# Optimization experiments

Hardware: AMD Instinct MI355X
Metric: run time of the kernel (lower is better)

Reference implementation:

```python
import jax, jax.numpy as jnp
import numpy as np

B, S, D, H = 4, 2048, 1024, 16
HD = D // H

def _linear_params(key, fan_in, fan_out):
    kw, kb = jax.random.split(key)
    bound = 1.0 / np.sqrt(fan_in)
    W = jax.random.uniform(kw, (fan_in, fan_out), minval=-bound, maxval=bound, dtype=jnp.float32)
    b = jax.random.uniform(kb, (fan_out,), minval=-bound, maxval=bound, dtype=jnp.float32)
    return W, b

def setup_inputs() -> dict:
    key = jax.random.key(0)
    ks = jax.random.split(key, 7)
    query = jax.random.normal(ks[0], (B, S, D), dtype=jnp.float32)
    key_t = jax.random.normal(ks[1], (B, S, D), dtype=jnp.float32)
    value = jax.random.normal(ks[2], (B, S, D), dtype=jnp.float32)
    Wq, bq = _linear_params(ks[3], D, D)
    Wk, bk = _linear_params(ks[4], D, D)
    Wv, bv = _linear_params(ks[5], D, D)
    Wo, bo = _linear_params(ks[6], D, D)
    return {"query": query, "key": key_t, "value": value,
            "Wq": Wq, "bq": bq, "Wk": Wk, "bk": bk,
            "Wv": Wv, "bv": bv, "Wo": Wo, "bo": bo}

def reference(query, key, value, Wq, bq, Wk, bk, Wv, bv, Wo, bo):
    b, s, _ = query.shape
    scale = HD ** -0.5
    # project and split heads -> [b, h, s, hd]
    Q = (query @ Wq + bq).reshape(b, s, H, HD).transpose(0, 2, 1, 3)
    K = (key @ Wk + bk).reshape(b, s, H, HD).transpose(0, 2, 1, 3)
    V = (value @ Wv + bv).reshape(b, s, H, HD).transpose(0, 2, 1, 3)
    scores = jnp.einsum('bhqd,bhkd->bhqk', Q, K) * scale  # [b,h,s,s]
    attn = jax.nn.softmax(scores, axis=-1)
    out = jnp.einsum('bhqk,bhkd->bhqd', attn, V)
    out = out.transpose(0, 2, 1, 3).reshape(b, s, D)
    return out @ Wo + bo
```

## Files before the change

### kernel.cpp

```cpp
#include <hip/hip_runtime.h>

typedef unsigned short u16;
typedef __attribute__((ext_vector_type(8))) short short8;
typedef __attribute__((ext_vector_type(4))) float f32x4;
typedef __attribute__((ext_vector_type(4))) unsigned int u32x4;

union V8 { u32x4 u; short8 s; };

__device__ __forceinline__ u16 f2bf(float f) {
  union { float f; unsigned u; } v; v.f = f;
  unsigned r = v.u + 0x7fffu + ((v.u >> 16) & 1u);
  return (u16)(r >> 16);
}

__device__ __forceinline__ unsigned cvt_pk_bf16(float lo, float hi) {
  unsigned r;
  asm("v_cvt_pk_bf16_f32 %0, %1, %2" : "=v"(r) : "v"(lo), "v"(hi));
  return r;
}

__device__ __forceinline__ void gload_lds16(const void* g, void* l) {
  __builtin_amdgcn_global_load_lds((const __attribute__((address_space(1))) unsigned int*)g,
                                   (__attribute__((address_space(3))) unsigned int*)l, 16, 0, 0);
}

__device__ __forceinline__ f32x4 mfma16(short8 a, short8 b, f32x4 c) {
  return __builtin_amdgcn_mfma_f32_16x16x32_bf16(a, b, c, 0, 0, 0);
}

__global__ __launch_bounds__(256) void wtrans4_kernel(const float* __restrict__ Wq, const float* __restrict__ Wk,
                                                      const float* __restrict__ Wv, const float* __restrict__ Wo,
                                                      u16* __restrict__ WtQ, u16* __restrict__ WtK,
                                                      u16* __restrict__ WtV, u16* __restrict__ WtO) {
  const int bid = blockIdx.x;
  const int wsel = bid >> 9;
  const float* W = (wsel == 0) ? Wq : (wsel == 1) ? Wk : (wsel == 2) ? Wv : Wo;
  u16* Wt = (wsel == 0) ? WtQ : (wsel == 1) ? WtK : (wsel == 2) ? WtV : WtO;
  const int tid = (bid & 511) * 256 + threadIdx.x;
  const int n = tid & 1023;
  const int kb = (tid >> 10) << 3;
  u32x4 w;
#pragma unroll
  for (int j = 0; j < 4; j++)
    w[j] = cvt_pk_bf16(W[(size_t)(kb + 2 * j) * 1024 + n], W[(size_t)(kb + 2 * j + 1) * 1024 + n]);
  *(u32x4*)(Wt + (size_t)n * 1024 + kb) = w;
}

__global__ __launch_bounds__(256) void gemm_qkv_kernel(const float* __restrict__ Aq,
                                                       const float* __restrict__ Ak,
                                                       const float* __restrict__ Av,
                                                       const u16* __restrict__ Wt,
                                                       const float* __restrict__ bq,
                                                       const float* __restrict__ bk,
                                                       const float* __restrict__ bv,
                                                       u16* __restrict__ Outs,
                                                       float qscale) {
  constexpr int K = 1024;
  __shared__ u16 Ash[2][4096];
  __shared__ u16 Bsh[2][4096];
  const int t = threadIdx.x;
  const int l = t & 63;
  const int w = t >> 6;
  const int wm = w >> 1, wn = w & 1;
  const int bid0 = blockIdx.x;
  const int swz = (bid0 & 7) * 192 + (bid0 >> 3);
  const int bm = swz >> 3, bn = swz & 7;
  const int sec = bm >> 6;
  const int m0 = (bm & 63) * 128, n0 = bn * 128;
  const float* Asrc = (sec == 0) ? Aq : (sec == 1) ? Ak : Av;
  const u16* Bb = Wt + ((size_t)sec << 20) + (size_t)n0 * K;

  f32x4 acc[4][4];
#pragma unroll
  for (int i = 0; i < 4; i++)
#pragma unroll
    for (int j = 0; j < 4; j++) acc[i][j] = (f32x4){0.f, 0.f, 0.f, 0.f};

  const int line0 = t >> 3, c8 = t & 7;
  const int lc0 = c8 ^ (line0 & 7);
  const int row0 = 2 * line0 + (lc0 >> 2);
  const int kc0 = (lc0 & 3) << 3;
  const int line1 = line0 + 32;
  const int lc1 = c8 ^ (line1 & 7);
  const int row1 = 2 * line1 + (lc1 >> 2);
  const int kc1 = (lc1 & 3) << 3;

  const float* A0 = Asrc + (size_t)(m0 + row0) * K + kc0;
  const float* A1 = Asrc + (size_t)(m0 + row1) * K + kc1;

  int aoff[4], boff[4];
#pragma unroll
  for (int mt = 0; mt < 4; mt++) {
    int R = wm * 64 + mt * 16 + (l & 15);
    int cc = (((R & 1) << 2) + (l >> 4)) ^ ((R >> 1) & 7);
    aoff[mt] = (R >> 1) * 64 + cc * 8;
  }
#pragma unroll
  for (int nt = 0; nt < 4; nt++) {
    int R = wn * 64 + nt * 16 + (l & 15);
    int cc = (((R & 1) << 2) + (l >> 4)) ^ ((R >> 1) & 7);
    boff[nt] = (R >> 1) * 64 + cc * 8;
  }

  float4 La0, La1, La2, La3;
  auto loadA = [&](int k0) {
    La0 = *(const float4*)(A0 + k0);
    La1 = *(const float4*)(A0 + k0 + 4);
    La2 = *(const float4*)(A1 + k0);
    La3 = *(const float4*)(A1 + k0 + 4);
  };
  auto writeA = [&](int buf) {
    u32x4 w0, w1;
    w0[0] = cvt_pk_bf16(La0.x, La0.y); w0[1] = cvt_pk_bf16(La0.z, La0.w);
    w0[2] = cvt_pk_bf16(La1.x, La1.y); w0[3] = cvt_pk_bf16(La1.z, La1.w);
    w1[0] = cvt_pk_bf16(La2.x, La2.y); w1[1] = cvt_pk_bf16(La2.z, La2.w);
    w1[2] = cvt_pk_bf16(La3.x, La3.y); w1[3] = cvt_pk_bf16(La3.z, La3.w);
    *(u32x4*)&Ash[buf][t * 8] = w0;
    *(u32x4*)&Ash[buf][2048 + t * 8] = w1;
  };
  auto stB = [&](int buf, int k0) {
    u16* BW = &Bsh[buf][w * 512];
    gload_lds16(Bb + (size_t)row0 * K + k0 + kc0, BW);
    gload_lds16(Bb + (size_t)row1 * K + k0 + kc1, BW + 2048);
  };

  loadA(0);
  stB(0, 0);
  writeA(0);
  __syncthreads();

  int cur = 0;
  for (int k0 = 0; k0 < K; k0 += 32) {
    const bool nxt = (k0 + 32 < K);
    if (nxt) { loadA(k0 + 32); stB(cur ^ 1, k0 + 32); }
    short8 af[4], bfr[4];
#pragma unroll
    for (int mt = 0; mt < 4; mt++) af[mt] = *(const short8*)&Ash[cur][aoff[mt]];
#pragma unroll
    for (int nt = 0; nt < 4; nt++) bfr[nt] = *(const short8*)&Bsh[cur][boff[nt]];
    __builtin_amdgcn_s_setprio(1);
#pragma unroll
    for (int mt = 0; mt < 4; mt++)
#pragma unroll
      for (int nt = 0; nt < 4; nt++)
        acc[mt][nt] = mfma16(af[mt], bfr[nt], acc[mt][nt]);
    __builtin_amdgcn_s_setprio(0);
    if (nxt) writeA(cur ^ 1);
    __syncthreads();
    cur ^= 1;
  }

#pragma unroll
  for (int nt = 0; nt < 4; nt++) {
    const int n = n0 + wn * 64 + nt * 16 + (l & 15);
    const float bias = (sec == 0) ? bq[n] : (sec == 1) ? bk[n] : bv[n];
    if (sec < 2) {
      const float outscale = (sec == 0) ? qscale : 1.0f;
      u16* C = Outs + ((size_t)sec << 23);
#pragma unroll
      for (int mt = 0; mt < 4; mt++) {
        const int m = m0 + wm * 64 + mt * 16 + ((l >> 4) << 2);
#pragma unroll
        for (int r = 0; r < 4; r++)
          C[(size_t)(m + r) * 1024 + n] = f2bf((acc[mt][nt][r] + bias) * outscale);
      }
    } else {
      const int b2 = m0 >> 11;
      const int h2 = n >> 6, d = n & 63;
      u16* C = Outs + ((size_t)2 << 23);
#pragma unroll
      for (int mt = 0; mt < 4; mt++) {
        const int s0 = (m0 & 2047) + wm * 64 + mt * 16 + ((l >> 4) << 2);
        const int u = s0 & 63;
        const int pos = ((((u >> 2) & 3) + ((u >> 5) & 1) * 4) << 3) + ((u >> 4) & 1) * 4;
        const int sp = (s0 & ~63) + pos;
        ushort4 pk;
        pk.x = f2bf(acc[mt][nt][0] + bias);
        pk.y = f2bf(acc[mt][nt][1] + bias);
        pk.z = f2bf(acc[mt][nt][2] + bias);
        pk.w = f2bf(acc[mt][nt][3] + bias);
        *(ushort4*)(C + (((size_t)((b2 * 16 + h2) * 64 + d)) << 11) + sp) = pk;
      }
    }
  }
}

__global__ __launch_bounds__(256) void gemm_out_kernel(const u16* __restrict__ A,
                                                       const u16* __restrict__ Bt,
                                                       const float* __restrict__ bias,
                                                       float* __restrict__ Cout) {
  constexpr int K = 1024;
  __shared__ u16 Ash[2][4096];
  __shared__ u16 Bsh[2][4096];
  const int t = threadIdx.x;
  const int l = t & 63;
  const int w = t >> 6;
  const int wm = w >> 1, wn = w & 1;
  const int bid0 = blockIdx.x;
  const int swz = (bid0 & 7) * 64 + (bid0 >> 3);
  const int bm = swz >> 3, bn = swz & 7;
  const int m0 = bm * 128, n0 = bn * 128;

  f32x4 acc[4][4];
#pragma unroll
  for (int i = 0; i < 4; i++)
#pragma unroll
    for (int j = 0; j < 4; j++) acc[i][j] = (f32x4){0.f, 0.f, 0.f, 0.f};

  const int line0 = t >> 3, c8 = t & 7;
  const int lc0 = c8 ^ (line0 & 7);
  const int row0 = 2 * line0 + (lc0 >> 2);
  const int kc0 = (lc0 & 3) << 3;
  const int line1 = line0 + 32;
  const int lc1 = c8 ^ (line1 & 7);
  const int row1 = 2 * line1 + (lc1 >> 2);
  const int kc1 = (lc1 & 3) << 3;

  const u16* Ab = A + (size_t)m0 * K;
  const u16* Bb = Bt + (size_t)n0 * K;

  int aoff[4], boff[4];
#pragma unroll
  for (int mt = 0; mt < 4; mt++) {
    int R = wm * 64 + mt * 16 + (l & 15);
    int cc = (((R & 1) << 2) + (l >> 4)) ^ ((R >> 1) & 7);
    aoff[mt] = (R >> 1) * 64 + cc * 8;
  }
#pragma unroll
  for (int nt = 0; nt < 4; nt++) {
    int R = wn * 64 + nt * 16 + (l & 15);
    int cc = (((R & 1) << 2) + (l >> 4)) ^ ((R >> 1) & 7);
    boff[nt] = (R >> 1) * 64 + cc * 8;
  }

  auto stage = [&](int buf, int k0) {
    u16* AW = &Ash[buf][w * 512];
    u16* BW = &Bsh[buf][w * 512];
    gload_lds16(Ab + (size_t)row0 * K + k0 + kc0, AW);
    gload_lds16(Ab + (size_t)row1 * K + k0 + kc1, AW + 2048);
    gload_lds16(Bb + (size_t)row0 * K + k0 + kc0, BW);
    gload_lds16(Bb + (size_t)row1 * K + k0 + kc1, BW + 2048);
  };

  stage(0, 0);
  __syncthreads();
  int cur = 0;
  for (int k0 = 0; k0 < K; k0 += 32) {
    if (k0 + 32 < K) stage(cur ^ 1, k0 + 32);
    short8 af[4], bfr[4];
#pragma unroll
    for (int mt = 0; mt < 4; mt++) af[mt] = *(const short8*)&Ash[cur][aoff[mt]];
#pragma unroll
    for (int nt = 0; nt < 4; nt++) bfr[nt] = *(const short8*)&Bsh[cur][boff[nt]];
    __builtin_amdgcn_s_setprio(1);
#pragma unroll
    for (int mt = 0; mt < 4; mt++)
#pragma unroll
      for (int nt = 0; nt < 4; nt++)
        acc[mt][nt] = mfma16(af[mt], bfr[nt], acc[mt][nt]);
    __builtin_amdgcn_s_setprio(0);
    __syncthreads();
    cur ^= 1;
  }

#pragma unroll
  for (int nt = 0; nt < 4; nt++) {
    const int n = n0 + wn * 64 + nt * 16 + (l & 15);
    const float bv2 = bias[n];
#pragma unroll
    for (int mt = 0; mt < 4; mt++) {
      const int m = m0 + wm * 64 + mt * 16 + ((l >> 4) << 2);
#pragma unroll
      for (int r = 0; r < 4; r++)
        Cout[(size_t)(m + r) * 1024 + n] = acc[mt][nt][r] + bv2;
    }
  }
}

__device__ __forceinline__ void pack_half(const f32x4 (&s)[4], short8& pa0, short8& pa1) {
  float p[4][4];
#pragma unroll
  for (int c = 0; c < 4; c++)
#pragma unroll
    for (int r = 0; r < 4; r++) p[c][r] = __builtin_amdgcn_exp2f(s[c][r]);
  V8 u0, u1;
  u0.u[0] = cvt_pk_bf16(p[0][0], p[0][1]); u0.u[1] = cvt_pk_bf16(p[0][2], p[0][3]);
  u0.u[2] = cvt_pk_bf16(p[1][0], p[1][1]); u0.u[3] = cvt_pk_bf16(p[1][2], p[1][3]);
  u1.u[0] = cvt_pk_bf16(p[2][0], p[2][1]); u1.u[1] = cvt_pk_bf16(p[2][2], p[2][3]);
  u1.u[2] = cvt_pk_bf16(p[3][0], p[3][1]); u1.u[3] = cvt_pk_bf16(p[3][2], p[3][3]);
  pa0 = u0.s; pa1 = u1.s;
}

__global__ __launch_bounds__(256, 2) void attn_kernel(const u16* __restrict__ Qb,
                                                      const u16* __restrict__ Kb,
                                                      const u16* __restrict__ Vtb,
                                                      u16* __restrict__ AO) {
  __shared__ u16 Ksh[2][4096];
  __shared__ u16 Vsh[2][4096];
  const int t = threadIdx.x, l = t & 63, w = t >> 6;
  const int g = l >> 4, ql = l & 15;
  const int bid0 = blockIdx.x;
  const int bid = (bid0 & 7) * 64 + (bid0 >> 3);
  const int qt = bid & 7;
  const int bh = bid >> 3;
  const int h = bh & 15, b = bh >> 4;
  const int q0 = qt * 256 + w * 64;

  short8 qf[4][2];
#pragma unroll
  for (int hh = 0; hh < 4; hh++) {
    const u16* Qrow = Qb + ((size_t)b * 2048 + q0 + hh * 16 + ql) * 1024 + h * 64 + g * 8;
    qf[hh][0] = *(const short8*)(Qrow);
    qf[hh][1] = *(const short8*)(Qrow + 32);
  }

  f32x4 oacc[4][4];
  f32x4 lacc[4];
#pragma unroll
  for (int hh = 0; hh < 4; hh++) {
    lacc[hh] = (f32x4){0.f, 0.f, 0.f, 0.f};
#pragma unroll
    for (int dt = 0; dt < 4; dt++) oacc[hh][dt] = (f32x4){0.f, 0.f, 0.f, 0.f};
  }
  short8 ones;
#pragma unroll
  for (int i = 0; i < 8; i++) ones[i] = (short)0x3F80;

  const int srow0 = t >> 3, sc = t & 7;
  const int slc0 = sc ^ (srow0 & 7);
  const int srow1 = srow0 + 32, slc1 = sc ^ (srow1 & 7);
  const u16* Kbase = Kb + ((size_t)b * 2048) * 1024 + h * 64;
  const u16* Vbase = Vtb + ((size_t)(b * 16 + h) * 64) * 2048;

  auto stage = [&](int buf, int kk0) {
    u16* KW = &Ksh[buf][w * 512];
    u16* VW = &Vsh[buf][w * 512];
    gload_lds16(Kbase + (size_t)(kk0 + srow0) * 1024 + slc0 * 8, KW);
    gload_lds16(Kbase + (size_t)(kk0 + srow1) * 1024 + slc1 * 8, KW + 2048);
    gload_lds16(Vbase + (size_t)srow0 * 2048 + kk0 + slc0 * 8, VW);
    gload_lds16(Vbase + (size_t)srow1 * 2048 + kk0 + slc1 * 8, VW + 2048);
  };

  int voff0[4], voff1[4];
#pragma unroll
  for (int dt = 0; dt < 4; dt++) {
    const int d = dt * 16 + ql;
    voff0[dt] = d * 64 + ((g ^ (d & 7)) << 3);
    voff1[dt] = d * 64 + (((g + 4) ^ (d & 7)) << 3);
  }

  stage(0, 0);
  __syncthreads();
  int cur = 0;

  for (int kk0 = 0; kk0 < 2048; kk0 += 64) {
    if (kk0 + 64 < 2048) stage(cur ^ 1, kk0 + 64);
    const u16* KC = Ksh[cur];
    const u16* VC = Vsh[cur];

    f32x4 s[4][4];
    __builtin_amdgcn_s_setprio(1);
#pragma unroll
    for (int c = 0; c < 4; c++) {
      const int R = c * 16 + ql;
      const int x = R & 7;
      const short8 kf0 = *(const short8*)&KC[R * 64 + ((g ^ x) << 3)];
      const short8 kf1 = *(const short8*)&KC[R * 64 + (((g + 4) ^ x) << 3)];
#pragma unroll
      for (int hh = 0; hh < 4; hh++) {
        f32x4 z = (f32x4){0.f, 0.f, 0.f, 0.f};
        z = mfma16(kf0, qf[hh][0], z);
        s[hh][c] = mfma16(kf1, qf[hh][1], z);
      }
    }
    __builtin_amdgcn_s_setprio(0);

    short8 pa[4][2];
#pragma unroll
    for (int hh = 0; hh < 4; hh++) pack_half(s[hh], pa[hh][0], pa[hh][1]);

    __builtin_amdgcn_s_setprio(1);
#pragma unroll
    for (int hh = 0; hh < 4; hh++) {
      lacc[hh] = mfma16(pa[hh][0], ones, lacc[hh]);
      lacc[hh] = mfma16(pa[hh][1], ones, lacc[hh]);
    }
#pragma unroll
    for (int dt = 0; dt < 4; dt++) {
      const short8 vf0 = *(const short8*)&VC[voff0[dt]];
      const short8 vf1 = *(const short8*)&VC[voff1[dt]];
#pragma unroll
      for (int hh = 0; hh < 4; hh++) {
        oacc[hh][dt] = mfma16(pa[hh][0], vf0, oacc[hh][dt]);
        oacc[hh][dt] = mfma16(pa[hh][1], vf1, oacc[hh][dt]);
      }
    }
    __builtin_amdgcn_s_setprio(0);
    __syncthreads();
    cur ^= 1;
  }

#pragma unroll
  for (int hh = 0; hh < 4; hh++) {
    f32x4 inv;
#pragma unroll
    for (int r = 0; r < 4; r++) inv[r] = __builtin_amdgcn_rcpf(lacc[hh][r]);
    u16* Arow = AO + ((size_t)b * 2048 + q0 + hh * 16) * 1024 + h * 64;
#pragma unroll
    for (int dt = 0; dt < 4; dt++) {
      const int col = dt * 16 + ql;
#pragma unroll
      for (int r = 0; r < 4; r++)
        Arow[(size_t)(4 * g + r) * 1024 + col] = f2bf(oacc[hh][dt][r] * inv[r]);
    }
  }
}

extern "C" void kernel_launch(void* const* d_in, const int* in_sizes, int n_in,
                              void* d_out, int out_size, void* d_ws, size_t ws_size,
                              hipStream_t stream) {
  (void)in_sizes; (void)n_in; (void)out_size; (void)ws_size;
  const float* query = (const float*)d_in[0];
  const float* key   = (const float*)d_in[1];
  const float* value = (const float*)d_in[2];
  const float* Wq = (const float*)d_in[3];  const float* bq = (const float*)d_in[4];
  const float* Wk = (const float*)d_in[5];  const float* bk = (const float*)d_in[6];
  const float* Wv = (const float*)d_in[7];  const float* bv = (const float*)d_in[8];
  const float* Wo = (const float*)d_in[9];  const float* bo = (const float*)d_in[10];
  float* out = (float*)d_out;

  const size_t SZX = (size_t)8192 * 1024;
  const size_t SZW = (size_t)1024 * 1024;
  u16* AO  = (u16*)d_ws;
  u16* Qb  = AO + SZX;
  u16* Kbf = Qb + SZX;
  u16* Vtb = Kbf + SZX;
  u16* WtQ = Vtb + SZX;
  u16* WtK = WtQ + SZW;
  u16* WtV = WtK + SZW;
  u16* WtO = WtV + SZW;

  const float QSCALE = 0.125f * 1.44269504088896f;

  wtrans4_kernel<<<2048, 256, 0, stream>>>(Wq, Wk, Wv, Wo, WtQ, WtK, WtV, WtO);

  gemm_qkv_kernel<<<1536, 256, 0, stream>>>(query, key, value, WtQ, bq, bk, bv, Qb, QSCALE);

  attn_kernel<<<512, 256, 0, stream>>>(Qb, Kbf, Vtb, AO);

  gemm_out_kernel<<<512, 256, 0, stream>>>(AO, WtO, bo, out);
}
```

Baseline: 369.5 us.

## Pre-convert QKV activations to bf16 and stage GEMM A via direct LDS loads

Adds a prep pass that converts the fp32 query/key/value inputs to bf16 in workspace, fused with the weight transpose kernel. The QKV GEMM then loads A through global_load_lds like B, dropping the register round-trip and in-loop conversion. It also removes the s_setprio hints in both GEMMs. The cost is an extra full read and write of the activations (about 48MB read, 24MB write) before the GEMM, traded for a simpler, fully asynchronous GEMM pipeline.

```diff
diff --git a/kernel.cpp b/kernel.cpp
--- a/kernel.cpp
+++ b/kernel.cpp
@@ -28,27 +28,42 @@
   return __builtin_amdgcn_mfma_f32_16x16x32_bf16(a, b, c, 0, 0, 0);
 }
 
-__global__ __launch_bounds__(256) void wtrans4_kernel(const float* __restrict__ Wq, const float* __restrict__ Wk,
-                                                      const float* __restrict__ Wv, const float* __restrict__ Wo,
-                                                      u16* __restrict__ WtQ, u16* __restrict__ WtK,
-                                                      u16* __restrict__ WtV, u16* __restrict__ WtO) {
+__global__ __launch_bounds__(256) void prep_kernel(const float* __restrict__ q,
+                                                   const float* __restrict__ k,
+                                                   const float* __restrict__ v,
+                                                   const float* __restrict__ Wq, const float* __restrict__ Wk,
+                                                   const float* __restrict__ Wv, const float* __restrict__ Wo,
+                                                   u16* __restrict__ oq, u16* __restrict__ ok, u16* __restrict__ ov,
+                                                   u16* __restrict__ WtQ, u16* __restrict__ WtK,
+                                                   u16* __restrict__ WtV, u16* __restrict__ WtO) {
   const int bid = blockIdx.x;
-  const int wsel = bid >> 9;
-  const float* W = (wsel == 0) ? Wq : (wsel == 1) ? Wk : (wsel == 2) ? Wv : Wo;
-  u16* Wt = (wsel == 0) ? WtQ : (wsel == 1) ? WtK : (wsel == 2) ? WtV : WtO;
-  const int tid = (bid & 511) * 256 + threadIdx.x;
-  const int n = tid & 1023;
-  const int kb = (tid >> 10) << 3;
-  u32x4 w;
-#pragma unroll
-  for (int j = 0; j < 4; j++)
-    w[j] = cvt_pk_bf16(W[(size_t)(kb + 2 * j) * 1024 + n], W[(size_t)(kb + 2 * j + 1) * 1024 + n]);
-  *(u32x4*)(Wt + (size_t)n * 1024 + kb) = w;
-}
-
-__global__ __launch_bounds__(256) void gemm_qkv_kernel(const float* __restrict__ Aq,
-                                                       const float* __restrict__ Ak,
-                                                       const float* __restrict__ Av,
+  if (bid < 12288) {
+    const float* in = (bid < 4096) ? q : (bid < 8192 ? k : v);
+    u16* out = (bid < 4096) ? oq : (bid < 8192 ? ok : ov);
+    const size_t i = ((size_t)(bid & 4095) * 256 + threadIdx.x) * 8;
+    const float4* p = (const float4*)(in + i);
+    float4 a = p[0], b = p[1];
+    u32x4 w;
+    w[0] = cvt_pk_bf16(a.x, a.y); w[1] = cvt_pk_bf16(a.z, a.w);
+    w[2] = cvt_pk_bf16(b.x, b.y); w[3] = cvt_pk_bf16(b.z, b.w);
+    *(u32x4*)(out + i) = w;
+  } else {
+    const int wb = bid - 12288;
+    const int wsel = wb >> 9;
+    const float* W = (wsel == 0) ? Wq : (wsel == 1) ? Wk : (wsel == 2) ? Wv : Wo;
+    u16* Wt = (wsel == 0) ? WtQ : (wsel == 1) ? WtK : (wsel == 2) ? WtV : WtO;
+    const int tid = (wb & 511) * 256 + threadIdx.x;
+    const int n = tid & 1023;
+    const int kb = (tid >> 10) << 3;
+    u32x4 w;
+#pragma unroll
+    for (int j = 0; j < 4; j++)
+      w[j] = cvt_pk_bf16(W[(size_t)(kb + 2 * j) * 1024 + n], W[(size_t)(kb + 2 * j + 1) * 1024 + n]);
+    *(u32x4*)(Wt + (size_t)n * 1024 + kb) = w;
+  }
+}
+
+__global__ __launch_bounds__(256) void gemm_qkv_kernel(const u16* __restrict__ A,
                                                        const u16* __restrict__ Wt,
                                                        const float* __restrict__ bq,
                                                        const float* __restrict__ bk,
@@ -65,10 +80,11 @@
   const int bid0 = blockIdx.x;
   const int swz = (bid0 & 7) * 192 + (bid0 >> 3);
   const int bm = swz >> 3, bn = swz & 7;
-  const int sec = bm >> 6;
-  const int m0 = (bm & 63) * 128, n0 = bn * 128;
-  const float* Asrc = (sec == 0) ? Aq : (sec == 1) ? Ak : Av;
-  const u16* Bb = Wt + ((size_t)sec << 20) + (size_t)n0 * K;
+  const int m0 = bm * 128, n0 = bn * 128;
+  const int sec = m0 >> 13;
+  const u16* Bt = Wt + ((size_t)sec << 20);
+  const float* bias = (sec == 0) ? bq : (sec == 1) ? bk : bv;
+  const float outscale = (sec == 0) ? qscale : 1.0f;
 
   f32x4 acc[4][4];
 #pragma unroll
@@ -85,8 +101,8 @@
   const int row1 = 2 * line1 + (lc1 >> 2);
   const int kc1 = (lc1 & 3) << 3;
 
-  const float* A0 = Asrc + (size_t)(m0 + row0) * K + kc0;
-  const float* A1 = Asrc + (size_t)(m0 + row1) * K + kc1;
+  const u16* Ab = A + (size_t)m0 * K;
+  const u16* Bb = Bt + (size_t)n0 * K;
 
   int aoff[4], boff[4];
 #pragma unroll
@@ -102,50 +118,30 @@
     boff[nt] = (R >> 1) * 64 + cc * 8;
   }
 
-  float4 La0, La1, La2, La3;
-  auto loadA = [&](int k0) {
-    La0 = *(const float4*)(A0 + k0);
-    La1 = *(const float4*)(A0 + k0 + 4);
-    La2 = *(const float4*)(A1 + k0);
-    La3 = *(const float4*)(A1 + k0 + 4);
-  };
-  auto writeA = [&](int buf) {
-    u32x4 w0, w1;
-    w0[0] = cvt_pk_bf16(La0.x, La0.y); w0[1] = cvt_pk_bf16(La0.z, La0.w);
-    w0[2] = cvt_pk_bf16(La1.x, La1.y); w0[3] = cvt_pk_bf16(La1.z, La1.w);
-    w1[0] = cvt_pk_bf16(La2.x, La2.y); w1[1] = cvt_pk_bf16(La2.z, La2.w);
-    w1[2] = cvt_pk_bf16(La3.x, La3.y); w1[3] = cvt_pk_bf16(La3.z, La3.w);
-    *(u32x4*)&Ash[buf][t * 8] = w0;
-    *(u32x4*)&Ash[buf][2048 + t * 8] = w1;
-  };
-  auto stB = [&](int buf, int k0) {
+  auto stage = [&](int buf, int k0) {
+    u16* AW = &Ash[buf][w * 512];
     u16* BW = &Bsh[buf][w * 512];
+    gload_lds16(Ab + (size_t)row0 * K + k0 + kc0, AW);
+    gload_lds16(Ab + (size_t)row1 * K + k0 + kc1, AW + 2048);
     gload_lds16(Bb + (size_t)row0 * K + k0 + kc0, BW);
     gload_lds16(Bb + (size_t)row1 * K + k0 + kc1, BW + 2048);
   };
 
-  loadA(0);
-  stB(0, 0);
-  writeA(0);
+  stage(0, 0);
   __syncthreads();
-
   int cur = 0;
   for (int k0 = 0; k0 < K; k0 += 32) {
-    const bool nxt = (k0 + 32 < K);
-    if (nxt) { loadA(k0 + 32); stB(cur ^ 1, k0 + 32); }
+    if (k0 + 32 < K) stage(cur ^ 1, k0 + 32);
     short8 af[4], bfr[4];
 #pragma unroll
     for (int mt = 0; mt < 4; mt++) af[mt] = *(const short8*)&Ash[cur][aoff[mt]];
 #pragma unroll
     for (int nt = 0; nt < 4; nt++) bfr[nt] = *(const short8*)&Bsh[cur][boff[nt]];
-    __builtin_amdgcn_s_setprio(1);
 #pragma unroll
     for (int mt = 0; mt < 4; mt++)
 #pragma unroll
       for (int nt = 0; nt < 4; nt++)
         acc[mt][nt] = mfma16(af[mt], bfr[nt], acc[mt][nt]);
-    __builtin_amdgcn_s_setprio(0);
-    if (nxt) writeA(cur ^ 1);
     __syncthreads();
     cur ^= 1;
   }
@@ -153,32 +149,32 @@
 #pragma unroll
   for (int nt = 0; nt < 4; nt++) {
     const int n = n0 + wn * 64 + nt * 16 + (l & 15);
-    const float bias = (sec == 0) ? bq[n] : (sec == 1) ? bk[n] : bv[n];
+    const float bv2 = bias[n];
     if (sec < 2) {
-      const float outscale = (sec == 0) ? qscale : 1.0f;
       u16* C = Outs + ((size_t)sec << 23);
 #pragma unroll
       for (int mt = 0; mt < 4; mt++) {
-        const int m = m0 + wm * 64 + mt * 16 + ((l >> 4) << 2);
+        const int m = (m0 & 8191) + wm * 64 + mt * 16 + ((l >> 4) << 2);
 #pragma unroll
         for (int r = 0; r < 4; r++)
-          C[(size_t)(m + r) * 1024 + n] = f2bf((acc[mt][nt][r] + bias) * outscale);
+          C[(size_t)(m + r) * 1024 + n] = f2bf((acc[mt][nt][r] + bv2) * outscale);
       }
     } else {
-      const int b2 = m0 >> 11;
+      const int mloc = m0 & 8191;
+      const int b2 = mloc >> 11;
       const int h2 = n >> 6, d = n & 63;
       u16* C = Outs + ((size_t)2 << 23);
 #pragma unroll
       for (int mt = 0; mt < 4; mt++) {
-        const int s0 = (m0 & 2047) + wm * 64 + mt * 16 + ((l >> 4) << 2);
+        const int s0 = (mloc & 2047) + wm * 64 + mt * 16 + ((l >> 4) << 2);
         const int u = s0 & 63;
         const int pos = ((((u >> 2) & 3) + ((u >> 5) & 1) * 4) << 3) + ((u >> 4) & 1) * 4;
         const int sp = (s0 & ~63) + pos;
         ushort4 pk;
-        pk.x = f2bf(acc[mt][nt][0] + bias);
-        pk.y = f2bf(acc[mt][nt][1] + bias);
-        pk.z = f2bf(acc[mt][nt][2] + bias);
-        pk.w = f2bf(acc[mt][nt][3] + bias);
+        pk.x = f2bf(acc[mt][nt][0] + bv2);
+        pk.y = f2bf(acc[mt][nt][1] + bv2);
+        pk.z = f2bf(acc[mt][nt][2] + bv2);
+        pk.w = f2bf(acc[mt][nt][3] + bv2);
         *(ushort4*)(C + (((size_t)((b2 * 16 + h2) * 64 + d)) << 11) + sp) = pk;
       }
     }
@@ -252,13 +248,11 @@
     for (int mt = 0; mt < 4; mt++) af[mt] = *(const short8*)&Ash[cur][aoff[mt]];
 #pragma unroll
     for (int nt = 0; nt < 4; nt++) bfr[nt] = *(const short8*)&Bsh[cur][boff[nt]];
-    __builtin_amdgcn_s_setprio(1);
 #pragma unroll
     for (int mt = 0; mt < 4; mt++)
 #pragma unroll
       for (int nt = 0; nt < 4; nt++)
         acc[mt][nt] = mfma16(af[mt], bfr[nt], acc[mt][nt]);
-    __builtin_amdgcn_s_setprio(0);
     __syncthreads();
     cur ^= 1;
   }
@@ -431,20 +425,24 @@
 
   const size_t SZX = (size_t)8192 * 1024;
   const size_t SZW = (size_t)1024 * 1024;
-  u16* AO  = (u16*)d_ws;
-  u16* Qb  = AO + SZX;
+  u16* qin = (u16*)d_ws;
+  u16* kin = qin + SZX;
+  u16* vin = kin + SZX;
+  u16* Qb  = vin + SZX;
   u16* Kbf = Qb + SZX;
   u16* Vtb = Kbf + SZX;
   u16* WtQ = Vtb + SZX;
   u16* WtK = WtQ + SZW;
   u16* WtV = WtK + SZW;
   u16* WtO = WtV + SZW;
+  u16* AO  = qin;
 
   const float QSCALE = 0.125f * 1.44269504088896f;
 
-  wtrans4_kernel<<<2048, 256, 0, stream>>>(Wq, Wk, Wv, Wo, WtQ, WtK, WtV, WtO);
-
-  gemm_qkv_kernel<<<1536, 256, 0, stream>>>(query, key, value, WtQ, bq, bk, bv, Qb, QSCALE);
+  prep_kernel<<<14336, 256, 0, stream>>>(query, key, value, Wq, Wk, Wv, Wo,
+                                         qin, kin, vin, WtQ, WtK, WtV, WtO);
+
+  gemm_qkv_kernel<<<1536, 256, 0, stream>>>(qin, WtQ, bq, bk, bv, Qb, QSCALE);
 
   attn_kernel<<<512, 256, 0, stream>>>(Qb, Kbf, Vtb, AO);
 
```

Measured after the change: 321.7 us. 12.9% less time.
